# Kernel tuning notes

Hardware: AMD Instinct MI355X
Metric: run time of the kernel (lower is better)

The kernel has to match this reference:

```python
import jax, jax.numpy as jnp
import numpy as np

B, DIN, DH, DOUT = 256, 784, 512, 10


def _softplus(x):
    # matches torch.log(1.0 + torch.exp(x)) exactly
    return jnp.log(1.0 + jnp.exp(x))


def _kl(w_mu, w_sigma_sp, size_in):
    # compute_kl_loss(w_mu, diag_embed(softplus(w_sigma))) without materializing diag
    # w_mu: (in, out), w_sigma_sp: (out, in)
    trace = jnp.sum(w_sigma_sp, axis=1)            # (out,)
    mu_sq = jnp.sum(w_mu * w_mu, axis=0)           # (out,)
    logdet = jnp.sum(jnp.log(w_sigma_sp), axis=1)  # slogdet of diag = sum log diag
    return 0.5 * jnp.sum(trace + mu_sq - size_in - logdet)


def setup_inputs() -> dict:
    key = jax.random.key(0)
    ks = jax.random.split(key, 9)
    inp = {
        "x": jax.random.normal(ks[0], (B, DIN, 1), dtype=jnp.float32),
        "w_mu1": 5e-5 * jax.random.normal(ks[1], (DIN, DH), dtype=jnp.float32),
        "w_sigma1": jax.random.uniform(ks[2], (DH, DIN), minval=-12.0, maxval=-2.0, dtype=jnp.float32),
        "b_mu1": 5e-5 * jax.random.normal(ks[3], (DH, 1), dtype=jnp.float32),
        "b_sigma1": jax.random.uniform(ks[4], (DH,), minval=-12.0, maxval=-2.0, dtype=jnp.float32),
        "w_mu2": 5e-5 * jax.random.normal(ks[5], (DH, DOUT), dtype=jnp.float32),
        "w_sigma2": jax.random.uniform(ks[6], (DOUT, DH), minval=-12.0, maxval=-2.0, dtype=jnp.float32),
        "b_mu2": 5e-5 * jax.random.normal(ks[7], (DOUT, 1), dtype=jnp.float32),
        "b_sigma2": jax.random.uniform(ks[8], (DOUT,), minval=-12.0, maxval=-2.0, dtype=jnp.float32),
    }
    return inp


def reference(x, w_mu1, w_sigma1, b_mu1, b_sigma1, w_mu2, w_sigma2, b_mu2, b_sigma2):
    batch = x.shape[0]
    eye_h = jnp.eye(DH, dtype=x.dtype)
    eye_o = jnp.eye(DOUT, dtype=x.dtype)

    # ---- RVLinearlayer 1 (sigma_in = None) ----
    xv = x[..., 0]                                   # (B, DIN)
    mu1 = jnp.einsum('io,bi->bo', w_mu1, xv)[:, :, None] + b_mu1   # (B, DH, 1)
    Ws1 = _softplus(w_sigma1)                        # (DH, DIN)
    quad1 = jnp.einsum('hi,bi->bh', Ws1, xv * xv)    # mu_in^T diag(Ws) mu_in per unit
    sigma1 = quad1[:, :, None] * eye_h + jnp.diag(_softplus(b_sigma1))  # (B, DH, DH)
    kl1 = _kl(w_mu1, Ws1, DIN)

    # ---- RVNonLinearFunc (ReLU) ----
    mu2 = jax.nn.relu(mu1)                           # (B, DH, 1)
    g = (mu1[..., 0] > 0).astype(x.dtype)            # Heaviside grad of relu
    sigma2 = sigma1 * (g[:, :, None] * g[:, None, :])

    # ---- RVLinearlayer 2 (with sigma_in) ----
    m2v = mu2[..., 0]                                # (B, DH)
    mu3 = jnp.einsum('ho,bh->bo', w_mu2, m2v)[:, :, None] + b_mu2   # (B, DOUT, 1)
    Ws2 = _softplus(w_sigma2)                        # (DOUT, DH)
    quad2 = jnp.einsum('oh,bh->bo', Ws2, m2v * m2v)  # (B, DOUT)
    # faithful replication of W_Sigma.view(out,-1) @ sigma_in.view(-1,B) then .view(B,out)
    Sflat = sigma2.reshape(DH * DH, batch)           # same row-major view as torch
    diag_rows = Sflat[jnp.arange(DH) * (DH + 1)]     # rows of the diag positions, (DH, B)
    tr = (Ws2 @ diag_rows).reshape(batch, DOUT)      # (out,B) -> row-major (B,out)
    mid = jnp.einsum('ho,bhk,kp->bop', w_mu2, sigma2, w_mu2)  # w_mu2^T Sigma w_mu2
    sigma3 = (tr[:, :, None] * eye_o + mid + quad2[:, :, None] * eye_o
              + jnp.diag(_softplus(b_sigma2)))       # (B, DOUT, DOUT)
    kl2 = _kl(w_mu2, Ws2, DH)

    # ---- RVSoftmax ----
    p = jax.nn.softmax(mu3[..., 0], axis=1)          # (B, DOUT)
    jac = p[:, :, None] * eye_o - p[:, :, None] * p[:, None, :]  # diag(p) - p p^T
    Sigma_out = jnp.einsum('bij,bjk,blk->bil', jac, sigma3, jac)

    return p, Sigma_out, kl1 + kl2
```

## Files before the change

### kernel.cpp

```cpp
#include <hip/hip_runtime.h>
#include <math.h>

#define BATCH 256
#define DIN 784
#define DH 512
#define DOUT 10
#define SPLITS 16
#define KSPL 49

__device__ __forceinline__ float softplus(float x) {
  return __logf(1.0f + __expf(x));
}

__global__ __launch_bounds__(256) void gemm1_kernel(
    const float* __restrict__ x, const float* __restrict__ w_mu1,
    const float* __restrict__ w_sigma1, const float* __restrict__ w_mu2,
    const float* __restrict__ w_sigma2, float* __restrict__ mu_part,
    float* __restrict__ q_part, float* __restrict__ kl_part) {
  __shared__ float xs[64][50];
  __shared__ float wmt[50][68];
  __shared__ float wst[50][68];
  __shared__ float rlds[4];
  const int t = threadIdx.x;
  const int h0 = blockIdx.x * 64;
  const int b0 = blockIdx.y * 64;
  const int s = blockIdx.z;
  const int i0 = s * KSPL;
  const int hl = (t & 15) * 4;
  const int bg = (t >> 4) * 4;

  for (int f = t; f < 64 * KSPL; f += 256) {
    const int bb = f / KSPL, kk = f - bb * KSPL;
    xs[bb][kk] = x[(b0 + bb) * DIN + i0 + kk];
  }
  for (int f = t; f < KSPL * 64; f += 256) {
    const int kk = f >> 6, hh = f & 63;
    wmt[kk][hh] = w_mu1[(i0 + kk) * DH + h0 + hh];
  }
  for (int f = t; f < 64 * KSPL; f += 256) {
    const int hh = f / KSPL, kk = f - hh * KSPL;
    wst[kk][hh] = softplus(w_sigma1[(h0 + hh) * DIN + i0 + kk]);
  }
  if (t < 64) {
    xs[t][49] = 0.f;
    wmt[49][t] = 0.f;
    wst[49][t] = 0.f;
  }
  __syncthreads();

  float mu[4][4], qq[4][4];
#pragma unroll
  for (int j = 0; j < 4; j++)
#pragma unroll
    for (int i = 0; i < 4; i++) {
      mu[j][i] = 0.f;
      qq[j][i] = 0.f;
    }

#pragma unroll 5
  for (int kk = 0; kk < 50; kk += 2) {
    const float4 wm0 = *(const float4*)&wmt[kk][hl];
    const float4 wm1 = *(const float4*)&wmt[kk + 1][hl];
    const float4 ws0 = *(const float4*)&wst[kk][hl];
    const float4 ws1 = *(const float4*)&wst[kk + 1][hl];
    const float* wm0a = (const float*)&wm0;
    const float* wm1a = (const float*)&wm1;
    const float* ws0a = (const float*)&ws0;
    const float* ws1a = (const float*)&ws1;
#pragma unroll
    for (int j = 0; j < 4; j++) {
      const float2 xv = *(const float2*)&xs[bg + j][kk];
      const float xx = xv.x, xy = xv.y;
      const float x2 = xx * xx, y2 = xy * xy;
#pragma unroll
      for (int i = 0; i < 4; i++) {
        mu[j][i] = fmaf(wm0a[i], xx, mu[j][i]);
        mu[j][i] = fmaf(wm1a[i], xy, mu[j][i]);
        qq[j][i] = fmaf(ws0a[i], x2, qq[j][i]);
        qq[j][i] = fmaf(ws1a[i], y2, qq[j][i]);
      }
    }
  }

  const int h = h0 + hl;
  const size_t base = (size_t)s * (BATCH * DH);
#pragma unroll
  for (int j = 0; j < 4; j++) {
    const size_t row = base + (size_t)(b0 + bg + j) * DH + h;
    *(float4*)&mu_part[row] = make_float4(mu[j][0], mu[j][1], mu[j][2], mu[j][3]);
    *(float4*)&q_part[row] = make_float4(qq[j][0], qq[j][1], qq[j][2], qq[j][3]);
  }

  float kl = 0.f;
  int slot = -1;
  if (blockIdx.y == 0) {
    for (int f = t; f < KSPL * 64; f += 256) {
      const int kk = f >> 6, hh = f & 63;
      const float sv = wst[kk][hh];
      kl += sv - __logf(sv);
    }
    slot = blockIdx.x * 16 + s;
  } else if (blockIdx.y == 1) {
    for (int f = t; f < KSPL * 64; f += 256) {
      const int kk = f >> 6, hh = f & 63;
      const float wv = wmt[kk][hh];
      kl = fmaf(wv, wv, kl);
    }
    slot = 128 + blockIdx.x * 16 + s;
  } else if (blockIdx.y == 2 && blockIdx.x == 0) {
    for (int idx = s * 320 + t; idx < s * 320 + 320; idx += 256) {
      const float sv = softplus(w_sigma2[idx]);
      const float wv = w_mu2[idx];
      kl += sv - __logf(sv);
      kl = fmaf(wv, wv, kl);
    }
    slot = 256 + s;
  }

  for (int off = 32; off > 0; off >>= 1) kl += __shfl_down(kl, off);
  const int lane = t & 63, wv = t >> 6;
  if (lane == 0) rlds[wv] = kl;
  __syncthreads();
  if (t == 0 && slot >= 0)
    kl_part[slot] = rlds[0] + rlds[1] + rlds[2] + rlds[3];
}

__global__ __launch_bounds__(256) void layer2_kernel(
    const float* __restrict__ mu_part, const float* __restrict__ q_part,
    const float* __restrict__ b_mu1, const float* __restrict__ b_sigma1,
    const float* __restrict__ w_mu2, const float* __restrict__ w_sigma2,
    const float* __restrict__ b_mu2, const float* __restrict__ b_sigma2,
    const float* __restrict__ kl_part, float* __restrict__ out_p,
    float* __restrict__ out_sigma, float* __restrict__ out_kl) {
  const int b = blockIdx.x, t = threadIdx.x;
  __shared__ float smu[DH], sq[DH];
  __shared__ float red[4][75];
  __shared__ float fin[75];
  __shared__ float mu3[10], pvec[10], trv[10], spb2[10];
  __shared__ float sig[10][10], Tm[10][10], cs[10], rs[10];
  __shared__ float klred[4];

  {
    const int arr = t >> 7;
    const int h4 = (t & 127) * 4;
    const float* srcbase = (arr == 0 ? mu_part : q_part);
    const float4* src = (const float4*)(srcbase + (size_t)b * DH + h4);
    float4 a = make_float4(0.f, 0.f, 0.f, 0.f);
#pragma unroll
    for (int s2 = 0; s2 < SPLITS; s2++) {
      const float4 v = src[(size_t)s2 * (BATCH * DH / 4)];
      a.x += v.x;
      a.y += v.y;
      a.z += v.z;
      a.w += v.w;
    }
    float* dst = (arr == 0 ? smu : sq);
    *(float4*)&dst[h4] = a;
  }
  __syncthreads();

  float m2v[2], d2v[2];
  {
    const float ma0 = smu[t] + b_mu1[t];
    const float ma1 = smu[t + 256] + b_mu1[t + 256];
    m2v[0] = ma0 > 0.f ? ma0 : 0.f;
    m2v[1] = ma1 > 0.f ? ma1 : 0.f;
    d2v[0] = ma0 > 0.f ? (sq[t] + softplus(b_sigma1[t])) : 0.f;
    d2v[1] = ma1 > 0.f ? (sq[t + 256] + softplus(b_sigma1[t + 256])) : 0.f;
  }

  float acc[75];
#pragma unroll
  for (int i = 0; i < 75; i++) acc[i] = 0.f;

#pragma unroll
  for (int hh = 0; hh < 2; hh++) {
    const int h = t + hh * 256;
    const float m2h = m2v[hh], d2h = d2v[hh];
    const float msq = m2h * m2h;
    float wrow[10];
#pragma unroll
    for (int o = 0; o < 10; o++) wrow[o] = w_mu2[h * 10 + o];
#pragma unroll
    for (int o = 0; o < 10; o++) {
      acc[o] = fmaf(wrow[o], m2h, acc[o]);
      acc[10 + o] = fmaf(softplus(w_sigma2[o * DH + h]), msq, acc[10 + o]);
    }
    int idx = 20;
#pragma unroll
    for (int o = 0; o < 10; o++) {
      const float wd = wrow[o] * d2h;
#pragma unroll
      for (int p = o; p < 10; p++) {
        acc[idx] = fmaf(wd, wrow[p], acc[idx]);
        idx++;
      }
    }
  }

  const int lane = t & 63, wv = t >> 6;
#pragma unroll
  for (int j = 0; j < 75; j++) {
    float v = acc[j];
    for (int off = 32; off > 0; off >>= 1) v += __shfl_down(v, off);
    if (lane == 0) red[wv][j] = v;
  }
  __syncthreads();
  if (t < 75) fin[t] = red[0][t] + red[1][t] + red[2][t] + red[3][t];
  __syncthreads();

  if (t < 10) {
    mu3[t] = fin[t] + b_mu2[t];
    spb2[t] = softplus(b_sigma2[t]);
    const int c0 = b * 10 + t;
    const int o2 = c0 >> 8, cc = c0 & 255;
    float mua = b_mu1[cc], qa = 0.f;
    float mub = b_mu1[256 + cc], qb = 0.f;
#pragma unroll
    for (int s2 = 0; s2 < SPLITS; s2++) {
      const size_t base = (size_t)s2 * (BATCH * DH) + (size_t)cc * DH;
      mua += mu_part[base + cc];
      qa += q_part[base + cc];
      mub += mu_part[base + 256 + cc];
      qb += q_part[base + 256 + cc];
    }
    const float d2aa = mua > 0.f ? (qa + softplus(b_sigma1[cc])) : 0.f;
    const float d2bb = mub > 0.f ? (qb + softplus(b_sigma1[256 + cc])) : 0.f;
    trv[t] = softplus(w_sigma2[o2 * DH + 2 * cc]) * d2aa +
             softplus(w_sigma2[o2 * DH + 2 * cc + 1]) * d2bb;
  }
  __syncthreads();

  if (t == 0) {
    float mx = mu3[0];
#pragma unroll
    for (int o = 1; o < 10; o++) mx = fmaxf(mx, mu3[o]);
    float e[10], se = 0.f;
#pragma unroll
    for (int o = 0; o < 10; o++) {
      e[o] = expf(mu3[o] - mx);
      se += e[o];
    }
    const float inv = 1.f / se;
#pragma unroll
    for (int o = 0; o < 10; o++) pvec[o] = e[o] * inv;
  }
  __syncthreads();

  if (t < 100) {
    const int o = t / 10, p = t % 10;
    const int i0 = o < p ? o : p, j0 = o < p ? p : o;
    const int idx = 10 * i0 - (i0 * (i0 - 1)) / 2 + (j0 - i0);
    float v = fin[20 + idx];
    if (o == p) v += trv[o] + fin[10 + o] + spb2[o];
    sig[o][p] = v;
  }
  __syncthreads();

  if (t < 10) {
    float s = 0.f;
#pragma unroll
    for (int j = 0; j < 10; j++) s = fmaf(pvec[j], sig[j][t], s);
    cs[t] = s;
  }
  __syncthreads();

  if (t < 100) {
    const int o = t / 10, p = t % 10;
    Tm[o][p] = pvec[o] * (sig[o][p] - cs[p]);
  }
  __syncthreads();

  if (t < 10) {
    float s = 0.f;
#pragma unroll
    for (int k = 0; k < 10; k++) s = fmaf(Tm[t][k], pvec[k], s);
    rs[t] = s;
  }
  __syncthreads();

  if (t < 100) {
    const int o = t / 10, p = t % 10;
    out_sigma[b * 100 + t] = pvec[p] * (Tm[o][p] - rs[o]);
  }
  if (t < 10) out_p[b * 10 + t] = pvec[t];

  float klv = 0.f;
  if (b == 0) {
    klv = kl_part[t];
    if (t < 16) klv += kl_part[256 + t];
  }
  for (int off = 32; off > 0; off >>= 1) klv += __shfl_down(klv, off);
  if (lane == 0) klred[wv] = klv;
  __syncthreads();
  if (b == 0 && t == 0) {
    out_kl[0] =
        0.5f * (klred[0] + klred[1] + klred[2] + klred[3] - 406528.0f);
  }
}

extern "C" void kernel_launch(void* const* d_in, const int* in_sizes, int n_in,
                              void* d_out, int out_size, void* d_ws,
                              size_t ws_size, hipStream_t stream) {
  const float* x = (const float*)d_in[0];
  const float* w_mu1 = (const float*)d_in[1];
  const float* w_sigma1 = (const float*)d_in[2];
  const float* b_mu1 = (const float*)d_in[3];
  const float* b_sigma1 = (const float*)d_in[4];
  const float* w_mu2 = (const float*)d_in[5];
  const float* w_sigma2 = (const float*)d_in[6];
  const float* b_mu2 = (const float*)d_in[7];
  const float* b_sigma2 = (const float*)d_in[8];

  float* out = (float*)d_out;
  float* out_p = out;
  float* out_sigma = out + 2560;
  float* out_kl = out + 28160;

  float* ws = (float*)d_ws;
  float* mu_part = ws;
  float* q_part = ws + SPLITS * BATCH * DH;
  float* kl_part = ws + 2 * SPLITS * BATCH * DH;

  gemm1_kernel<<<dim3(8, 4, 16), 256, 0, stream>>>(
      x, w_mu1, w_sigma1, w_mu2, w_sigma2, mu_part, q_part, kl_part);
  layer2_kernel<<<256, 256, 0, stream>>>(mu_part, q_part, b_mu1, b_sigma1,
                                         w_mu2, w_sigma2, b_mu2, b_sigma2,
                                         kl_part, out_p, out_sigma, out_kl);
}
```

Before: 122.3 us.

## Increase K-split to 28 and widen layer2 to 512 threads per batch row

The first GEMM's K dimension is split into 28 chunks of 28 instead of 16 of 49, which raises the grid to 896 blocks for better CU coverage and drops the padding column. The layer2 kernel now runs 512 threads, one hidden unit per thread, with the partial-sum reduction split across two halves. The trace diagonal gather is parallelized over 70 threads instead of 10 serial loops. The trade-off is more partial-sum traffic through the workspace (28 slices to write and re-read) and a larger layer2 block.

```diff
diff --git a/kernel.cpp b/kernel.cpp
--- a/kernel.cpp
+++ b/kernel.cpp
@@ -5,8 +5,8 @@
 #define DIN 784
 #define DH 512
 #define DOUT 10
-#define SPLITS 16
-#define KSPL 49
+#define SPLITS 28
+#define KSPL 28
 
 __device__ __forceinline__ float softplus(float x) {
   return __logf(1.0f + __expf(x));
@@ -17,9 +17,9 @@
     const float* __restrict__ w_sigma1, const float* __restrict__ w_mu2,
     const float* __restrict__ w_sigma2, float* __restrict__ mu_part,
     float* __restrict__ q_part, float* __restrict__ kl_part) {
-  __shared__ float xs[64][50];
-  __shared__ float wmt[50][68];
-  __shared__ float wst[50][68];
+  __shared__ float xs[64][KSPL];
+  __shared__ float wmt[KSPL][68];
+  __shared__ float wst[KSPL][68];
   __shared__ float rlds[4];
   const int t = threadIdx.x;
   const int h0 = blockIdx.x * 64;
@@ -41,11 +41,6 @@
     const int hh = f / KSPL, kk = f - hh * KSPL;
     wst[kk][hh] = softplus(w_sigma1[(h0 + hh) * DIN + i0 + kk]);
   }
-  if (t < 64) {
-    xs[t][49] = 0.f;
-    wmt[49][t] = 0.f;
-    wst[49][t] = 0.f;
-  }
   __syncthreads();
 
   float mu[4][4], qq[4][4];
@@ -57,8 +52,8 @@
       qq[j][i] = 0.f;
     }
 
-#pragma unroll 5
-  for (int kk = 0; kk < 50; kk += 2) {
+#pragma unroll 7
+  for (int kk = 0; kk < KSPL; kk += 2) {
     const float4 wm0 = *(const float4*)&wmt[kk][hl];
     const float4 wm1 = *(const float4*)&wmt[kk + 1][hl];
     const float4 ws0 = *(const float4*)&wst[kk][hl];
@@ -87,8 +82,10 @@
 #pragma unroll
   for (int j = 0; j < 4; j++) {
     const size_t row = base + (size_t)(b0 + bg + j) * DH + h;
-    *(float4*)&mu_part[row] = make_float4(mu[j][0], mu[j][1], mu[j][2], mu[j][3]);
-    *(float4*)&q_part[row] = make_float4(qq[j][0], qq[j][1], qq[j][2], qq[j][3]);
+    *(float4*)&mu_part[row] =
+        make_float4(mu[j][0], mu[j][1], mu[j][2], mu[j][3]);
+    *(float4*)&q_part[row] =
+        make_float4(qq[j][0], qq[j][1], qq[j][2], qq[j][3]);
   }
 
   float kl = 0.f;
@@ -99,22 +96,22 @@
       const float sv = wst[kk][hh];
       kl += sv - __logf(sv);
     }
-    slot = blockIdx.x * 16 + s;
+    slot = blockIdx.x * 28 + s;
   } else if (blockIdx.y == 1) {
     for (int f = t; f < KSPL * 64; f += 256) {
       const int kk = f >> 6, hh = f & 63;
       const float wv = wmt[kk][hh];
       kl = fmaf(wv, wv, kl);
     }
-    slot = 128 + blockIdx.x * 16 + s;
-  } else if (blockIdx.y == 2 && blockIdx.x == 0) {
+    slot = 224 + blockIdx.x * 28 + s;
+  } else if (blockIdx.y == 2 && blockIdx.x == 0 && s < 16) {
     for (int idx = s * 320 + t; idx < s * 320 + 320; idx += 256) {
       const float sv = softplus(w_sigma2[idx]);
       const float wv = w_mu2[idx];
       kl += sv - __logf(sv);
       kl = fmaf(wv, wv, kl);
     }
-    slot = 256 + s;
+    slot = 448 + s;
   }
 
   for (int off = 32; off > 0; off >>= 1) kl += __shfl_down(kl, off);
@@ -125,7 +122,7 @@
     kl_part[slot] = rlds[0] + rlds[1] + rlds[2] + rlds[3];
 }
 
-__global__ __launch_bounds__(256) void layer2_kernel(
+__global__ __launch_bounds__(512) void layer2_kernel(
     const float* __restrict__ mu_part, const float* __restrict__ q_part,
     const float* __restrict__ b_mu1, const float* __restrict__ b_sigma1,
     const float* __restrict__ w_mu2, const float* __restrict__ w_sigma2,
@@ -133,50 +130,62 @@
     const float* __restrict__ kl_part, float* __restrict__ out_p,
     float* __restrict__ out_sigma, float* __restrict__ out_kl) {
   const int b = blockIdx.x, t = threadIdx.x;
-  __shared__ float smu[DH], sq[DH];
-  __shared__ float red[4][75];
+  __shared__ float smuA[DH], sqA[DH], smuB[DH], sqB[DH];
+  __shared__ float4 trp[10][7];
+  __shared__ float red[8][75];
   __shared__ float fin[75];
   __shared__ float mu3[10], pvec[10], trv[10], spb2[10];
   __shared__ float sig[10][10], Tm[10][10], cs[10], rs[10];
-  __shared__ float klred[4];
+  __shared__ float klred[8];
 
   {
-    const int arr = t >> 7;
+    const int half = t >> 8;
+    const int arr = (t >> 7) & 1;
     const int h4 = (t & 127) * 4;
     const float* srcbase = (arr == 0 ? mu_part : q_part);
     const float4* src = (const float4*)(srcbase + (size_t)b * DH + h4);
     float4 a = make_float4(0.f, 0.f, 0.f, 0.f);
 #pragma unroll
-    for (int s2 = 0; s2 < SPLITS; s2++) {
+    for (int s2 = half * 14; s2 < half * 14 + 14; s2++) {
       const float4 v = src[(size_t)s2 * (BATCH * DH / 4)];
       a.x += v.x;
       a.y += v.y;
       a.z += v.z;
       a.w += v.w;
     }
-    float* dst = (arr == 0 ? smu : sq);
+    float* dst = (half == 0 ? (arr == 0 ? smuA : sqA)
+                            : (arr == 0 ? smuB : sqB));
     *(float4*)&dst[h4] = a;
   }
-  __syncthreads();
-
-  float m2v[2], d2v[2];
+
+  if (t < 70) {
+    const int o = t / 7, g = t % 7;
+    const int cc = (b * 10 + o) & 255;
+    float mua = 0.f, qa = 0.f, mub = 0.f, qb = 0.f;
+#pragma unroll
+    for (int s2 = 4 * g; s2 < 4 * g + 4; s2++) {
+      const size_t base = (size_t)s2 * (BATCH * DH) + (size_t)cc * DH;
+      mua += mu_part[base + cc];
+      qa += q_part[base + cc];
+      mub += mu_part[base + 256 + cc];
+      qb += q_part[base + 256 + cc];
+    }
+    trp[o][g] = make_float4(mua, qa, mub, qb);
+  }
+  __syncthreads();
+
+  const int h = t;
+  float m2h, d2h;
   {
-    const float ma0 = smu[t] + b_mu1[t];
-    const float ma1 = smu[t + 256] + b_mu1[t + 256];
-    m2v[0] = ma0 > 0.f ? ma0 : 0.f;
-    m2v[1] = ma1 > 0.f ? ma1 : 0.f;
-    d2v[0] = ma0 > 0.f ? (sq[t] + softplus(b_sigma1[t])) : 0.f;
-    d2v[1] = ma1 > 0.f ? (sq[t + 256] + softplus(b_sigma1[t + 256])) : 0.f;
+    const float ma = smuA[h] + smuB[h] + b_mu1[h];
+    m2h = ma > 0.f ? ma : 0.f;
+    d2h = ma > 0.f ? (sqA[h] + sqB[h] + softplus(b_sigma1[h])) : 0.f;
   }
 
   float acc[75];
 #pragma unroll
   for (int i = 0; i < 75; i++) acc[i] = 0.f;
-
-#pragma unroll
-  for (int hh = 0; hh < 2; hh++) {
-    const int h = t + hh * 256;
-    const float m2h = m2v[hh], d2h = d2v[hh];
+  {
     const float msq = m2h * m2h;
     float wrow[10];
 #pragma unroll
@@ -206,7 +215,12 @@
     if (lane == 0) red[wv][j] = v;
   }
   __syncthreads();
-  if (t < 75) fin[t] = red[0][t] + red[1][t] + red[2][t] + red[3][t];
+  if (t < 75) {
+    float v = 0.f;
+#pragma unroll
+    for (int w = 0; w < 8; w++) v += red[w][t];
+    fin[t] = v;
+  }
   __syncthreads();
 
   if (t < 10) {
@@ -217,12 +231,12 @@
     float mua = b_mu1[cc], qa = 0.f;
     float mub = b_mu1[256 + cc], qb = 0.f;
 #pragma unroll
-    for (int s2 = 0; s2 < SPLITS; s2++) {
-      const size_t base = (size_t)s2 * (BATCH * DH) + (size_t)cc * DH;
-      mua += mu_part[base + cc];
-      qa += q_part[base + cc];
-      mub += mu_part[base + 256 + cc];
-      qb += q_part[base + 256 + cc];
+    for (int g = 0; g < 7; g++) {
+      const float4 v = trp[t][g];
+      mua += v.x;
+      qa += v.y;
+      mub += v.z;
+      qb += v.w;
     }
     const float d2aa = mua > 0.f ? (qa + softplus(b_sigma1[cc])) : 0.f;
     const float d2bb = mub > 0.f ? (qb + softplus(b_sigma1[256 + cc])) : 0.f;
@@ -238,7 +252,7 @@
     float e[10], se = 0.f;
 #pragma unroll
     for (int o = 0; o < 10; o++) {
-      e[o] = expf(mu3[o] - mx);
+      e[o] = __expf(mu3[o] - mx);
       se += e[o];
     }
     const float inv = 1.f / se;
@@ -285,17 +299,15 @@
   }
   if (t < 10) out_p[b * 10 + t] = pvec[t];
 
-  float klv = 0.f;
-  if (b == 0) {
-    klv = kl_part[t];
-    if (t < 16) klv += kl_part[256 + t];
-  }
+  float klv = (b == 0 && t < 464) ? kl_part[t] : 0.f;
   for (int off = 32; off > 0; off >>= 1) klv += __shfl_down(klv, off);
   if (lane == 0) klred[wv] = klv;
   __syncthreads();
   if (b == 0 && t == 0) {
-    out_kl[0] =
-        0.5f * (klred[0] + klred[1] + klred[2] + klred[3] - 406528.0f);
+    float s = 0.f;
+#pragma unroll
+    for (int w = 0; w < 8; w++) s += klred[w];
+    out_kl[0] = 0.5f * (s - 406528.0f);
   }
 }
 
@@ -322,9 +334,9 @@
   float* q_part = ws + SPLITS * BATCH * DH;
   float* kl_part = ws + 2 * SPLITS * BATCH * DH;
 
-  gemm1_kernel<<<dim3(8, 4, 16), 256, 0, stream>>>(
+  gemm1_kernel<<<dim3(8, 4, SPLITS), 256, 0, stream>>>(
       x, w_mu1, w_sigma1, w_mu2, w_sigma2, mu_part, q_part, kl_part);
-  layer2_kernel<<<256, 256, 0, stream>>>(mu_part, q_part, b_mu1, b_sigma1,
+  layer2_kernel<<<256, 512, 0, stream>>>(mu_part, q_part, b_mu1, b_sigma1,
                                          w_mu2, w_sigma2, b_mu2, b_sigma2,
                                          kl_part, out_p, out_sigma, out_kl);
 }
```

After: 116.9 us (median of 2 runs). 4.4% less time.
